# Kernel tuning notes

Hardware: AMD Instinct MI355X
Metric: run time of the kernel (lower is better)

## Reference

```python
import jax, jax.numpy as jnp
import numpy as np

B, IN, OUT, P = 512, 4096, 4096, 4
BITS = 4
MAX_INT = float(2 ** (BITS - 1) - 1)  # 7.0


def setup_inputs() -> dict:
    key = jax.random.key(0)
    k1, k2, k3, k4 = jax.random.split(key, 4)
    x = jax.random.normal(k1, (B, IN), dtype=jnp.float32)
    # Cached LFSR-generated pseudo-random matrix, values normalized to [-1, 1]
    U = jax.random.uniform(k2, (OUT * IN, P), dtype=jnp.float32, minval=-1.0, maxval=1.0)
    # 4-bit quantized projection: integers in [-7, 7] stored as float
    q = jnp.round(jnp.clip(jax.random.normal(k3, (P,), dtype=jnp.float32) * 3.0, -MAX_INT, MAX_INT))
    b = jax.random.normal(k4, (OUT,), dtype=jnp.float32)
    return {"x": x, "U": U, "q": q, "b": b, "exponent": 0}


def reference(x, U, q, b, exponent):
    # dequantize: t_hat = q / max_int * 2^exponent  (shared-exponent 4-bit dequant)
    scale = jnp.float32(2.0) ** exponent
    t_hat = q / MAX_INT * scale                      # [P]
    # reconstruct full weight: W = U @ t_hat, reshape to (out, in)
    w = (U @ t_hat).reshape(OUT, IN)                 # [OUT, IN]
    # original layer forward (nn.Linear): y = x @ W^T + b
    return x @ w.T + b                               # [B, OUT]
```

## Files before the change

kernel.cpp:

```cpp
#include <hip/hip_runtime.h>
#include <hip/hip_bf16.h>

typedef unsigned short ushort_t;
typedef unsigned int uint_t;
typedef __attribute__((ext_vector_type(4))) float f32x4;
typedef __attribute__((ext_vector_type(8))) short bf16x8;

#define B_DIM 512
#define IN_DIM 4096
#define OUT_DIM 4096
#define BM 128
#define BN 128
#define BK 32
#define KSPLIT 8

__device__ __forceinline__ ushort_t f2bf(float f) {
    union { float f; uint_t u; } v; v.f = f;
    uint_t r = v.u + 0x7fffu + ((v.u >> 16) & 1u);
    return (ushort_t)(r >> 16);
}

__device__ __forceinline__ void async_copy16(void* lds, const void* g) {
    __builtin_amdgcn_global_load_lds(
        (const __attribute__((address_space(1))) uint_t*)g,
        (__attribute__((address_space(3))) uint_t*)lds, 16, 0, 0);
}

__global__ __launch_bounds__(256) void build_w(const float4* __restrict__ U4,
                                               const float* __restrict__ q,
                                               const int* __restrict__ expo,
                                               ushort_t* __restrict__ Wb) {
    const float scale = exp2f((float)expo[0]) * (1.0f / 7.0f);
    const float t0 = q[0] * scale, t1 = q[1] * scale,
                t2 = q[2] * scale, t3 = q[3] * scale;
    size_t i = (size_t)blockIdx.x * 256 + threadIdx.x;
    float4 u = U4[i];
    Wb[i] = f2bf(u.x * t0 + u.y * t1 + u.z * t2 + u.w * t3);
}

__global__ __launch_bounds__(256) void conv_x(const float4* __restrict__ X4,
                                              ushort_t* __restrict__ Xb) {
    size_t i = (size_t)blockIdx.x * 256 + threadIdx.x;
    float4 a = X4[i];
    ushort_t r[4] = { f2bf(a.x), f2bf(a.y), f2bf(a.z), f2bf(a.w) };
    *(uint2*)(Xb + i * 4) = *(const uint2*)r;
}

__global__ __launch_bounds__(256, 4) void gemm_splitk(
    const ushort_t* __restrict__ A,
    const ushort_t* __restrict__ Bm,
    float* __restrict__ part)
{
    const int M = B_DIM, N = OUT_DIM, K = IN_DIM;
    __shared__ ushort_t sA[BM * BK];
    __shared__ ushort_t sB[BN * BK];

    const int tid  = threadIdx.x;
    const int lane = tid & 63;
    const int wave = tid >> 6;
    const int wr = (wave >> 1) * 64;
    const int wc = (wave & 1) * 64;

    const int m0 = blockIdx.y * BM;
    const int n0 = blockIdx.x * BN;
    const int kseg  = K / KSPLIT;
    const size_t kbase = (size_t)blockIdx.z * kseg;

    const int srow = tid >> 2;
    const int scol = (tid & 3) * 8;
    const ushort_t* ga0 = A  + (size_t)(m0 + srow) * K + kbase + scol;
    const ushort_t* ga1 = ga0 + (size_t)64 * K;
    const ushort_t* gb0 = Bm + (size_t)(n0 + srow) * K + kbase + scol;
    const ushort_t* gb1 = gb0 + (size_t)64 * K;
    ushort_t* la = sA + tid * 8;
    ushort_t* lb = sB + tid * 8;

    const int quad = lane >> 4;
    const int r16  = lane & 15;
    const ushort_t* fa = sA + (wr + r16) * BK + quad * 8;
    const ushort_t* fb = sB + (wc + r16) * BK + quad * 8;

    f32x4 acc[4][4] = {};

    const int nsteps = kseg / BK;
    for (int s = 0; s < nsteps; ++s) {
        async_copy16(la,        ga0);
        async_copy16(la + 2048, ga1);
        async_copy16(lb,        gb0);
        async_copy16(lb + 2048, gb1);
        ga0 += BK; ga1 += BK; gb0 += BK; gb1 += BK;
        __syncthreads();

        bf16x8 av[4], bv[4];
#pragma unroll
        for (int i = 0; i < 4; ++i) {
            av[i] = *(const bf16x8*)(fa + i * 16 * BK);
            bv[i] = *(const bf16x8*)(fb + i * 16 * BK);
        }
#pragma unroll
        for (int i = 0; i < 4; ++i)
#pragma unroll
            for (int j = 0; j < 4; ++j)
                acc[i][j] = __builtin_amdgcn_mfma_f32_16x16x32_bf16(
                    av[i], bv[j], acc[i][j], 0, 0, 0);
        __syncthreads();
    }

    float* outp = part + (size_t)blockIdx.z * M * N;
#pragma unroll
    for (int i = 0; i < 4; ++i) {
        const int mrow = m0 + wr + i * 16 + quad * 4;
#pragma unroll
        for (int j = 0; j < 4; ++j) {
            const int ncol = n0 + wc + j * 16 + r16;
            float* o = outp + (size_t)mrow * N + ncol;
#pragma unroll
            for (int r = 0; r < 4; ++r)
                o[(size_t)r * N] = acc[i][j][r];
        }
    }
}

__global__ __launch_bounds__(256) void reduce_bias(const float4* __restrict__ part,
                                                   const float4* __restrict__ bias,
                                                   float4* __restrict__ out) {
    const int MN4 = (B_DIM * OUT_DIM) / 4;
    int i = blockIdx.x * 256 + threadIdx.x;
    float4 bb = bias[i & 1023];
    float sx = bb.x, sy = bb.y, sz = bb.z, sw = bb.w;
#pragma unroll
    for (int k = 0; k < KSPLIT; ++k) {
        float4 p = part[i + (size_t)k * MN4];
        sx += p.x; sy += p.y; sz += p.z; sw += p.w;
    }
    float4 o; o.x = sx; o.y = sy; o.z = sz; o.w = sw;
    out[i] = o;
}

extern "C" void kernel_launch(void* const* d_in, const int* in_sizes, int n_in,
                              void* d_out, int out_size, void* d_ws, size_t ws_size,
                              hipStream_t stream) {
    const float* x    = (const float*)d_in[0];
    const float* U    = (const float*)d_in[1];
    const float* q    = (const float*)d_in[2];
    const float* b    = (const float*)d_in[3];
    const int*   expo = (const int*)d_in[4];
    float* out = (float*)d_out;

    char* ws = (char*)d_ws;
    ushort_t* Wb  = (ushort_t*)ws;
    ushort_t* Xb  = (ushort_t*)(ws + 33554432);
    float*    prt = (float*)(ws + 37748736);

    build_w<<<65536, 256, 0, stream>>>((const float4*)U, q, expo, Wb);
    conv_x<<<2048, 256, 0, stream>>>((const float4*)x, Xb);
    gemm_splitk<<<dim3(32, 4, KSPLIT), 256, 0, stream>>>(Xb, Wb, prt);
    reduce_bias<<<2048, 256, 0, stream>>>((const float4*)prt, (const float4*)b,
                                          (float4*)out);
}
```

Before: 415.5 us.

## Fuse weight reconstruction from U into split-K GEMM B-tile loading

Removes the separate build_w kernel and instead reads the fp32 U matrix inside the GEMM, projecting each group of four values by the dequantized t vector and storing bf16 results straight into LDS. Each block now covers all 512 batch rows with a 64-column N tile, so every weight element is built exactly once. This avoids writing and re-reading a 32MB bf16 weight buffer and one kernel launch. The trade-off is that the U loads are synchronous register loads in the main loop, with fewer blocks and lower occupancy to hide their latency.

```diff
diff --git a/kernel.cpp b/kernel.cpp
--- a/kernel.cpp
+++ b/kernel.cpp
@@ -9,8 +9,7 @@
 #define B_DIM 512
 #define IN_DIM 4096
 #define OUT_DIM 4096
-#define BM 128
-#define BN 128
+#define BN 64
 #define BK 32
 #define KSPLIT 8
 
@@ -26,18 +25,6 @@
         (__attribute__((address_space(3))) uint_t*)lds, 16, 0, 0);
 }
 
-__global__ __launch_bounds__(256) void build_w(const float4* __restrict__ U4,
-                                               const float* __restrict__ q,
-                                               const int* __restrict__ expo,
-                                               ushort_t* __restrict__ Wb) {
-    const float scale = exp2f((float)expo[0]) * (1.0f / 7.0f);
-    const float t0 = q[0] * scale, t1 = q[1] * scale,
-                t2 = q[2] * scale, t3 = q[3] * scale;
-    size_t i = (size_t)blockIdx.x * 256 + threadIdx.x;
-    float4 u = U4[i];
-    Wb[i] = f2bf(u.x * t0 + u.y * t1 + u.z * t2 + u.w * t3);
-}
-
 __global__ __launch_bounds__(256) void conv_x(const float4* __restrict__ X4,
                                               ushort_t* __restrict__ Xb) {
     size_t i = (size_t)blockIdx.x * 256 + threadIdx.x;
@@ -46,73 +33,85 @@
     *(uint2*)(Xb + i * 4) = *(const uint2*)r;
 }
 
-__global__ __launch_bounds__(256, 4) void gemm_splitk(
-    const ushort_t* __restrict__ A,
-    const ushort_t* __restrict__ Bm,
+__global__ __launch_bounds__(256, 2) void gemm_fused(
+    const ushort_t* __restrict__ Xb,
+    const float4* __restrict__ U4,
+    const float* __restrict__ q,
+    const int* __restrict__ expo,
     float* __restrict__ part)
 {
-    const int M = B_DIM, N = OUT_DIM, K = IN_DIM;
-    __shared__ ushort_t sA[BM * BK];
-    __shared__ ushort_t sB[BN * BK];
+    const int K = IN_DIM, N = OUT_DIM, M = B_DIM;
+    __shared__ ushort_t sX[512 * 32];
+    __shared__ ushort_t sU[64 * 32];
 
     const int tid  = threadIdx.x;
     const int lane = tid & 63;
     const int wave = tid >> 6;
-    const int wr = (wave >> 1) * 64;
-    const int wc = (wave & 1) * 64;
+    const int n0 = blockIdx.x * BN;
+    const int kz = blockIdx.y;
+    const int kseg = K / KSPLIT;
+    const size_t kbase = (size_t)kz * kseg;
 
-    const int m0 = blockIdx.y * BM;
-    const int n0 = blockIdx.x * BN;
-    const int kseg  = K / KSPLIT;
-    const size_t kbase = (size_t)blockIdx.z * kseg;
+    const float scale = exp2f((float)expo[0]) * (1.0f / 7.0f);
+    const float t0 = q[0] * scale, t1 = q[1] * scale,
+                t2 = q[2] * scale, t3 = q[3] * scale;
 
-    const int srow = tid >> 2;
-    const int scol = (tid & 3) * 8;
-    const ushort_t* ga0 = A  + (size_t)(m0 + srow) * K + kbase + scol;
-    const ushort_t* ga1 = ga0 + (size_t)64 * K;
-    const ushort_t* gb0 = Bm + (size_t)(n0 + srow) * K + kbase + scol;
-    const ushort_t* gb1 = gb0 + (size_t)64 * K;
-    ushort_t* la = sA + tid * 8;
-    ushort_t* lb = sB + tid * 8;
+    const int xrow = tid >> 2;
+    const int xcol = (tid & 3) * 8;
+    const ushort_t* gx = Xb + (size_t)xrow * K + kbase + xcol;
+    ushort_t* lx = sX + tid * 8;
+
+    const int nb = tid >> 4;
+    const int kp = tid & 15;
+    const float4* gu = U4 + (size_t)(n0 + nb) * K + kbase + 2 * kp;
+    uint_t* lu = (uint_t*)sU + nb * 16 + kp;
 
     const int quad = lane >> 4;
     const int r16  = lane & 15;
-    const ushort_t* fa = sA + (wr + r16) * BK + quad * 8;
-    const ushort_t* fb = sB + (wc + r16) * BK + quad * 8;
+    const ushort_t* fa = sX + (wave * 128 + r16) * 32 + quad * 8;
+    const ushort_t* fb = sU + r16 * 32 + quad * 8;
 
-    f32x4 acc[4][4] = {};
+    f32x4 acc[8][4] = {};
 
     const int nsteps = kseg / BK;
     for (int s = 0; s < nsteps; ++s) {
-        async_copy16(la,        ga0);
-        async_copy16(la + 2048, ga1);
-        async_copy16(lb,        gb0);
-        async_copy16(lb + 2048, gb1);
-        ga0 += BK; ga1 += BK; gb0 += BK; gb1 += BK;
+#pragma unroll
+        for (int p = 0; p < 8; ++p)
+            async_copy16(lx + p * 2048, gx + (size_t)p * 64 * K);
+        gx += BK;
+#pragma unroll
+        for (int r = 0; r < 4; ++r) {
+            const float4* g = gu + (size_t)r * 16 * K;
+            float4 ua = g[0], ub = g[1];
+            float w0 = ua.x * t0 + ua.y * t1 + ua.z * t2 + ua.w * t3;
+            float w1 = ub.x * t0 + ub.y * t1 + ub.z * t2 + ub.w * t3;
+            lu[r * 256] = (uint_t)f2bf(w0) | ((uint_t)f2bf(w1) << 16);
+        }
+        gu += BK;
         __syncthreads();
 
-        bf16x8 av[4], bv[4];
+        bf16x8 bv[4];
 #pragma unroll
-        for (int i = 0; i < 4; ++i) {
-            av[i] = *(const bf16x8*)(fa + i * 16 * BK);
-            bv[i] = *(const bf16x8*)(fb + i * 16 * BK);
-        }
+        for (int j = 0; j < 4; ++j)
+            bv[j] = *(const bf16x8*)(fb + j * 16 * 32);
 #pragma unroll
-        for (int i = 0; i < 4; ++i)
+        for (int i = 0; i < 8; ++i) {
+            bf16x8 av = *(const bf16x8*)(fa + i * 16 * 32);
 #pragma unroll
             for (int j = 0; j < 4; ++j)
                 acc[i][j] = __builtin_amdgcn_mfma_f32_16x16x32_bf16(
-                    av[i], bv[j], acc[i][j], 0, 0, 0);
+                    av, bv[j], acc[i][j], 0, 0, 0);
+        }
         __syncthreads();
     }
 
-    float* outp = part + (size_t)blockIdx.z * M * N;
+    float* outp = part + (size_t)kz * M * N;
 #pragma unroll
-    for (int i = 0; i < 4; ++i) {
-        const int mrow = m0 + wr + i * 16 + quad * 4;
+    for (int i = 0; i < 8; ++i) {
+        const int mrow = wave * 128 + i * 16 + quad * 4;
 #pragma unroll
         for (int j = 0; j < 4; ++j) {
-            const int ncol = n0 + wc + j * 16 + r16;
+            const int ncol = n0 + j * 16 + r16;
             float* o = outp + (size_t)mrow * N + ncol;
 #pragma unroll
             for (int r = 0; r < 4; ++r)
@@ -148,13 +147,12 @@
     float* out = (float*)d_out;
 
     char* ws = (char*)d_ws;
-    ushort_t* Wb  = (ushort_t*)ws;
-    ushort_t* Xb  = (ushort_t*)(ws + 33554432);
-    float*    prt = (float*)(ws + 37748736);
+    float*    prt = (float*)ws;
+    ushort_t* Xb  = (ushort_t*)(ws + 67108864);
 
-    build_w<<<65536, 256, 0, stream>>>((const float4*)U, q, expo, Wb);
     conv_x<<<2048, 256, 0, stream>>>((const float4*)x, Xb);
-    gemm_splitk<<<dim3(32, 4, KSPLIT), 256, 0, stream>>>(Xb, Wb, prt);
+    gemm_fused<<<dim3(64, KSPLIT), 256, 0, stream>>>(Xb, (const float4*)U,
+                                                     q, expo, prt);
     reduce_bias<<<2048, 256, 0, stream>>>((const float4*)prt, (const float4*)b,
                                           (float4*)out);
 }
```

Result: no change. 418.8 us (+0.8%).
